# Kernel optimization log

Hardware: AMD Instinct MI355X
Metric: run time of the kernel (lower is better)

Reference implementation:

```python
import jax, jax.numpy as jnp
import numpy as np

N = 50000      # nodes
E = 400000     # edges per hop
IN = 256       # in_channels
H = 4          # heads
C = 64         # out_channels per head
NEG = 0.2      # leaky relu negative slope


def setup_inputs() -> dict:
    key = jax.random.key(0)
    ks = jax.random.split(key, 10)
    x = jax.random.normal(ks[0], (N, IN), dtype=jnp.float32)
    edge_index1 = jax.random.randint(ks[1], (2, E), 0, N, dtype=jnp.int32)
    edge_index2 = jax.random.randint(ks[2], (2, E), 0, N, dtype=jnp.int32)
    s = 0.05
    Wl0 = jax.random.normal(ks[3], (IN, H * C), dtype=jnp.float32) * s
    Wr0 = jax.random.normal(ks[4], (IN, H * C), dtype=jnp.float32) * s
    att0 = jax.random.normal(ks[5], (H, C), dtype=jnp.float32) * s
    Wl1 = jax.random.normal(ks[6], (IN, H * C), dtype=jnp.float32) * s
    Wr1 = jax.random.normal(ks[7], (IN, H * C), dtype=jnp.float32) * s
    att1 = jax.random.normal(ks[8], (H, C), dtype=jnp.float32) * s
    return {"x": x, "Wl0": Wl0, "Wr0": Wr0, "att0": att0,
            "Wl1": Wl1, "Wr1": Wr1, "att1": att1,
            "edge_index1": edge_index1, "edge_index2": edge_index2}


def _gatv2_hop(x, Wl, Wr, att, src, dst):
    """One GATv2Conv hop (bias=False, residual=False, eval-mode dropout, concat=False)."""
    n = x.shape[0]
    xl = (x @ Wl).reshape(n, H, C)   # source-side projection
    xr = (x @ Wr).reshape(n, H, C)   # target-side projection
    # edge-wise GATv2 score: a^T leaky_relu(x_l[j] + x_r[i])
    m = jax.nn.leaky_relu(xl[src] + xr[dst], NEG)            # [E, H, C]
    e = jnp.einsum('ehc,hc->eh', m, att)                     # [E, H]
    # segment softmax over incoming edges of each destination node
    e_max = jax.lax.stop_gradient(
        jax.ops.segment_max(e, dst, num_segments=n))         # [N, H]
    ex = jnp.exp(e - e_max[dst])
    denom = jax.ops.segment_sum(ex, dst, num_segments=n)     # [N, H]
    alpha = ex / (denom[dst] + 1e-16)                        # [E, H]
    msg = xl[src] * alpha[:, :, None]                        # [E, H, C]
    out = jax.ops.segment_sum(msg, dst, num_segments=n)      # [N, H, C]
    return out.mean(axis=1)                                  # concat=False -> mean heads


def reference(x, Wl0, Wr0, att0, Wl1, Wr1, att1, edge_index1, edge_index2):
    n = x.shape[0]
    # hop 0: add_self_loops=True
    loop = jnp.arange(n, dtype=edge_index1.dtype)
    src0 = jnp.concatenate([edge_index1[0], loop])
    dst0 = jnp.concatenate([edge_index1[1], loop])
    out = _gatv2_hop(x, Wl0, Wr0, att0, src0, dst0)
    # hop 1: no self loops, scaled by 1/(k+1) = 1/2
    out = out + _gatv2_hop(x, Wl1, Wr1, att1, edge_index2[0], edge_index2[1]) / 2.0
    return out
```

## Files before the change

### kernel.cpp

```cpp
#include <hip/hip_runtime.h>

typedef unsigned int uint;
typedef unsigned short ushort;

typedef __bf16 bf16x8 __attribute__((ext_vector_type(8)));
typedef float f32x4 __attribute__((ext_vector_type(4)));

#define CAP 48

__device__ __forceinline__ float bf2f(ushort u) {
    return __uint_as_float(((uint)u) << 16);
}
__device__ __forceinline__ ushort f2bf(float f) {
    uint u = __float_as_uint(f);
    u += 0x7fffu + ((u >> 16) & 1u);
    return (ushort)(u >> 16);
}
__device__ __forceinline__ float4 up4(ushort4 v) {
    return make_float4(bf2f(v.x), bf2f(v.y), bf2f(v.z), bf2f(v.w));
}
__device__ __forceinline__ float lrelu(float v) {
    return v > 0.f ? v : 0.2f * v;
}
__device__ __forceinline__ void load_lds16(const ushort* g, ushort* l) {
    __builtin_amdgcn_global_load_lds(
        (const __attribute__((address_space(1))) void*)g,
        (__attribute__((address_space(3))) void*)l, 16, 0, 0);
}
__device__ __forceinline__ int swz(int row) { return (row + (row >> 2)) & 3; }

__global__ __launch_bounds__(256) void prep(
    const float* __restrict__ X, ushort* __restrict__ Xb, int Nrows, int Mpad,
    const float* __restrict__ Wl0, const float* __restrict__ Wr0,
    const float* __restrict__ Wl1, const float* __restrict__ Wr1,
    ushort* __restrict__ Wt,
    int* __restrict__ cnt0, int* __restrict__ srcs0, int* __restrict__ cnt1)
{
    const int BX = Mpad / 8;
    int blk = blockIdx.x;
    if (blk < BX) {
        int i = blk * 256 + threadIdx.x;
        int base = i * 8;
        int row = base >> 8;
        ushort o[8];
        if (row < Nrows) {
            float4 v0 = *(const float4*)(X + base);
            float4 v1 = *(const float4*)(X + base + 4);
            o[0] = f2bf(v0.x); o[1] = f2bf(v0.y); o[2] = f2bf(v0.z); o[3] = f2bf(v0.w);
            o[4] = f2bf(v1.x); o[5] = f2bf(v1.y); o[6] = f2bf(v1.z); o[7] = f2bf(v1.w);
        } else {
#pragma unroll
            for (int j = 0; j < 8; j++) o[j] = 0;
        }
        *(uint4*)(Xb + base) = *(const uint4*)o;
        return;
    }
    blk -= BX;
    if (blk < 1024) {
        int n = blk;
        int k = threadIdx.x;
        const float* W = (n < 256) ? Wl0 : (n < 512) ? Wr0 : (n < 768) ? Wl1 : Wr1;
        Wt[n * 256 + k] = f2bf(W[k * 256 + (n & 255)]);
        return;
    }
    blk -= 1024;
    int d = blk * 256 + threadIdx.x;
    if (d < Nrows) {
        cnt0[d] = 1;
        srcs0[(size_t)d * CAP] = d;
        cnt1[d] = 0;
    }
}

__global__ __launch_bounds__(256) void csr_scatter2(
    const int* __restrict__ ei1, const int* __restrict__ ei2,
    int* __restrict__ cnt0, int* __restrict__ srcs0,
    int* __restrict__ cnt1, int* __restrict__ srcs1,
    int E1, int E2)
{
    int e = blockIdx.x * 256 + threadIdx.x;
    if (e < E1) {
        int d = ei1[E1 + e];
        int pos = atomicAdd(&cnt0[d], 1);
        if (pos < CAP) srcs0[(size_t)d * CAP + pos] = ei1[e];
    } else if (e < E1 + E2) {
        int e2 = e - E1;
        int d = ei2[E2 + e2];
        int pos = atomicAdd(&cnt1[d], 1);
        if (pos < CAP) srcs1[(size_t)d * CAP + pos] = ei2[e2];
    }
}

__global__ __launch_bounds__(256, 2) void gemm_mfma(
    const ushort* __restrict__ Xb,
    const ushort* __restrict__ Wt,
    ushort* __restrict__ XP,
    int Nrows)
{
    __shared__ ushort As[128 * 32];
    __shared__ ushort Bs[128 * 32];

    const int tid = threadIdx.x;
    const int w = tid >> 6, l = tid & 63;
    const int wm = w & 1, wn = w >> 1;
    const int m0 = blockIdx.y * 128;
    const int n0g = blockIdx.x * 128;

    f32x4 acc[4][4];
#pragma unroll
    for (int i = 0; i < 4; i++)
#pragma unroll
        for (int j = 0; j < 4; j++) acc[i][j] = (f32x4)(0.f);

    const int fr = l & 15, fq = l >> 4;
    int a_off[4], b_off[4];
#pragma unroll
    for (int t = 0; t < 4; t++) {
        int rA = wm * 64 + t * 16 + fr;
        a_off[t] = (rA * 4 + ((fq + swz(rA)) & 3)) * 8;
        int rB = wn * 64 + t * 16 + fr;
        b_off[t] = (rB * 4 + ((fq + swz(rB)) & 3)) * 8;
    }

    for (int k0 = 0; k0 < 256; k0 += 32) {
        __syncthreads();
#pragma unroll
        for (int r = 0; r < 2; r++) {
            int slot = r * 256 + tid;
            int row = slot >> 2;
            int kp = ((slot & 3) - swz(row)) & 3;
            load_lds16(Xb + (size_t)(m0 + row) * 256 + k0 + kp * 8,
                       &As[(r * 256 + w * 64) * 8]);
            load_lds16(Wt + (size_t)(n0g + row) * 256 + k0 + kp * 8,
                       &Bs[(r * 256 + w * 64) * 8]);
        }
        __syncthreads();

        bf16x8 a[4], b[4];
#pragma unroll
        for (int t = 0; t < 4; t++) {
            a[t] = *(const bf16x8*)(As + a_off[t]);
            b[t] = *(const bf16x8*)(Bs + b_off[t]);
        }
#pragma unroll
        for (int mi = 0; mi < 4; mi++)
#pragma unroll
            for (int ni = 0; ni < 4; ni++)
                acc[mi][ni] = __builtin_amdgcn_mfma_f32_16x16x32_bf16(
                    a[mi], b[ni], acc[mi][ni], 0, 0, 0);
    }

    ushort* OUT = XP + (size_t)(n0g >> 8) * ((size_t)Nrows * 256);
    const int cbase = (n0g & 255) + wn * 64 + fr;
#pragma unroll
    for (int mi = 0; mi < 4; mi++) {
#pragma unroll
        for (int reg = 0; reg < 4; reg++) {
            int row = m0 + wm * 64 + mi * 16 + fq * 4 + reg;
            if (row >= Nrows) continue;
#pragma unroll
            for (int ni = 0; ni < 4; ni++) {
                OUT[(size_t)row * 256 + cbase + ni * 16] = f2bf(acc[mi][ni][reg]);
            }
        }
    }
}

__device__ __forceinline__ ushort4 gat_load(const ushort* __restrict__ XLb,
                                            int s, int lane) {
    return *(const ushort4*)(XLb + (size_t)s * 256 + lane * 4);
}
__device__ __forceinline__ void edge_accum(ushort4 raw, float4 xr, float4 av,
        float& a0, float& a1, float& a2, float& a3, float& den) {
    float4 xa = up4(raw);
    float p = av.x * lrelu(xa.x + xr.x) + av.y * lrelu(xa.y + xr.y)
            + av.z * lrelu(xa.z + xr.z) + av.w * lrelu(xa.w + xr.w);
    p += __shfl_xor(p, 1);
    p += __shfl_xor(p, 2);
    p += __shfl_xor(p, 4);
    p += __shfl_xor(p, 8);
    float exv = __expf(p);
    den += exv;
    a0 = fmaf(exv, xa.x, a0);
    a1 = fmaf(exv, xa.y, a1);
    a2 = fmaf(exv, xa.z, a2);
    a3 = fmaf(exv, xa.w, a3);
}

__global__ __launch_bounds__(256) void gat_aggregate(
    const ushort* __restrict__ XLb,
    const ushort* __restrict__ XRb,
    const float* __restrict__ att,
    const int* __restrict__ cnt,
    const int* __restrict__ srcs,
    const float* __restrict__ base,
    float* __restrict__ outp,
    float scale, int N)
{
    int d = blockIdx.x * 4 + (threadIdx.x >> 6);
    if (d >= N) return;
    int lane = threadIdx.x & 63;

    float4 xr = up4(*(const ushort4*)(XRb + (size_t)d * 256 + lane * 4));
    float4 av = *(const float4*)(att + lane * 4);

    int m = cnt[d];
    if (m > CAP) m = CAP;
    int sv = (lane < m) ? srcs[(size_t)d * CAP + lane] : 0;

    float a0 = 0.f, a1 = 0.f, a2 = 0.f, a3 = 0.f, den = 0.f;

    if (m > 0) {
        const int c = m - 1;
        ushort4 p[8];
#pragma unroll
        for (int j = 0; j < 8; j++)
            if (j <= c) p[j] = gat_load(XLb, __shfl(sv, j), lane);
        for (int i = 0; i < m; i += 8) {
            ushort4 cur[8];
#pragma unroll
            for (int j = 0; j < 8; j++) cur[j] = p[j];
            int b = i + 8;
#pragma unroll
            for (int j = 0; j < 8; j++)
                if (b + j <= c) p[j] = gat_load(XLb, __shfl(sv, b + j), lane);
#pragma unroll
            for (int j = 0; j < 8; j++)
                if (i + j < m) edge_accum(cur[j], xr, av, a0, a1, a2, a3, den);
        }
    }

    float inv = scale / (den + 1e-16f);
    float v0 = a0 * inv, v1 = a1 * inv, v2 = a2 * inv, v3 = a3 * inv;
    v0 += __shfl_xor(v0, 16); v0 += __shfl_xor(v0, 32);
    v1 += __shfl_xor(v1, 16); v1 += __shfl_xor(v1, 32);
    v2 += __shfl_xor(v2, 16); v2 += __shfl_xor(v2, 32);
    v3 += __shfl_xor(v3, 16); v3 += __shfl_xor(v3, 32);
    int jsel = lane >> 4;
    float vv = (jsel == 0) ? v0 : (jsel == 1) ? v1 : (jsel == 2) ? v2 : v3;
    int ch = ((lane & 15) << 2) + jsel;
    float prev = base ? base[(size_t)d * 64 + ch] : 0.f;
    outp[(size_t)d * 64 + ch] = prev + vv;
}

extern "C" void kernel_launch(void* const* d_in, const int* in_sizes, int n_in,
                              void* d_out, int out_size, void* d_ws, size_t ws_size,
                              hipStream_t stream)
{
    const float* x    = (const float*)d_in[0];
    const float* Wl0  = (const float*)d_in[1];
    const float* Wr0  = (const float*)d_in[2];
    const float* att0 = (const float*)d_in[3];
    const float* Wl1  = (const float*)d_in[4];
    const float* Wr1  = (const float*)d_in[5];
    const float* att1 = (const float*)d_in[6];
    const int* ei1 = (const int*)d_in[7];
    const int* ei2 = (const int*)d_in[8];

    const int N  = in_sizes[0] / 256;
    const int E1 = in_sizes[7] / 2;
    const int E2 = in_sizes[8] / 2;
    const int Mpad = ((N + 127) / 128) * 128;
    const size_t NB = (size_t)N * 256;

    char* ws = (char*)d_ws;
    size_t off = 0;
    ushort* Xb  = (ushort*)(ws + off); off += (size_t)Mpad * 256 * sizeof(ushort);
    ushort* Wt  = (ushort*)(ws + off); off += (size_t)1024 * 256 * sizeof(ushort);
    int* cnt0   = (int*)(ws + off);    off += (size_t)N * sizeof(int);
    int* cnt1   = (int*)(ws + off);    off += (size_t)N * sizeof(int);
    int* srcs0  = (int*)(ws + off);    off += (size_t)N * CAP * sizeof(int);
    int* srcs1  = (int*)(ws + off);    off += (size_t)N * CAP * sizeof(int);
    ushort* XP  = (ushort*)(ws + off);
    size_t need_mega = off + 4 * NB * sizeof(ushort);
    const bool mega = (ws_size >= need_mega);
    float* outf = (float*)d_out;

    const int BX = Mpad / 8;
    int prep_blocks = BX + 1024 + (N + 255) / 256;
    prep<<<prep_blocks, 256, 0, stream>>>(x, Xb, N, Mpad, Wl0, Wr0, Wl1, Wr1,
                                          Wt, cnt0, srcs0, cnt1);
    csr_scatter2<<<(E1 + E2 + 255) / 256, 256, 0, stream>>>(
        ei1, ei2, cnt0, srcs0, cnt1, srcs1, E1, E2);

    int aggblk = (N + 3) / 4;
    if (mega) {
        gemm_mfma<<<dim3(8, Mpad / 128), 256, 0, stream>>>(Xb, Wt, XP, N);
        gat_aggregate<<<aggblk, 256, 0, stream>>>(XP, XP + NB, att0, cnt0, srcs0,
                                                  nullptr, outf, 0.25f, N);
        gat_aggregate<<<aggblk, 256, 0, stream>>>(XP + 2 * NB, XP + 3 * NB, att1,
                                                  cnt1, srcs1, outf, outf, 0.125f, N);
    } else {
        gemm_mfma<<<dim3(4, Mpad / 128), 256, 0, stream>>>(Xb, Wt, XP, N);
        gat_aggregate<<<aggblk, 256, 0, stream>>>(XP, XP + NB, att0, cnt0, srcs0,
                                                  nullptr, outf, 0.25f, N);
        gemm_mfma<<<dim3(4, Mpad / 128), 256, 0, stream>>>(Xb, Wt + 512 * 256, XP, N);
        gat_aggregate<<<aggblk, 256, 0, stream>>>(XP, XP + NB, att1, cnt1, srcs1,
                                                  outf, outf, 0.125f, N);
    }
}
```

Before: 297.9 us.

## Fuse both GAT hops into one aggregation kernel with implicit self-loops

Merges the two per-hop aggregation kernels into a single kernel that computes hop 0 and hop 1 for each destination node and writes the output once. This removes a launch and the read-modify-write of the intermediate output. The self-loop is now handled as an implicit extra edge instead of being stored in the CSR, so hop 0's bucket cap no longer loses a slot to it. Other changes: the prefetch depth drops from 8 to 4 with masked tail edges instead of branches, the edge count is made wave-uniform via readfirstlane, and leaky-ReLU becomes fmax. In exchange, each wave carries more live registers across both hops.

```diff
diff --git a/kernel.cpp b/kernel.cpp
--- a/kernel.cpp
+++ b/kernel.cpp
@@ -18,9 +18,6 @@
 }
 __device__ __forceinline__ float4 up4(ushort4 v) {
     return make_float4(bf2f(v.x), bf2f(v.y), bf2f(v.z), bf2f(v.w));
-}
-__device__ __forceinline__ float lrelu(float v) {
-    return v > 0.f ? v : 0.2f * v;
 }
 __device__ __forceinline__ void load_lds16(const ushort* g, ushort* l) {
     __builtin_amdgcn_global_load_lds(
@@ -34,7 +31,7 @@
     const float* __restrict__ Wl0, const float* __restrict__ Wr0,
     const float* __restrict__ Wl1, const float* __restrict__ Wr1,
     ushort* __restrict__ Wt,
-    int* __restrict__ cnt0, int* __restrict__ srcs0, int* __restrict__ cnt1)
+    int* __restrict__ cnt0, int* __restrict__ cnt1)
 {
     const int BX = Mpad / 8;
     int blk = blockIdx.x;
@@ -66,8 +63,7 @@
     blk -= 1024;
     int d = blk * 256 + threadIdx.x;
     if (d < Nrows) {
-        cnt0[d] = 1;
-        srcs0[(size_t)d * CAP] = d;
+        cnt0[d] = 0;
         cnt1[d] = 0;
     }
 }
@@ -166,72 +162,106 @@
     }
 }
 
-__device__ __forceinline__ ushort4 gat_load(const ushort* __restrict__ XLb,
-                                            int s, int lane) {
-    return *(const ushort4*)(XLb + (size_t)s * 256 + lane * 4);
-}
-__device__ __forceinline__ void edge_accum(ushort4 raw, float4 xr, float4 av,
-        float& a0, float& a1, float& a2, float& a3, float& den) {
-    float4 xa = up4(raw);
-    float p = av.x * lrelu(xa.x + xr.x) + av.y * lrelu(xa.y + xr.y)
-            + av.z * lrelu(xa.z + xr.z) + av.w * lrelu(xa.w + xr.w);
+__device__ __forceinline__ void eacc(ushort4 raw, bool live,
+    const float4& xr, const float4& av,
+    float& a0, float& a1, float& a2, float& a3, float& den)
+{
+    float x0 = bf2f(raw.x), x1 = bf2f(raw.y), x2 = bf2f(raw.z), x3 = bf2f(raw.w);
+    float t0 = x0 + xr.x, t1 = x1 + xr.y, t2 = x2 + xr.z, t3 = x3 + xr.w;
+    float m0 = fmaxf(t0, 0.2f * t0), m1 = fmaxf(t1, 0.2f * t1);
+    float m2 = fmaxf(t2, 0.2f * t2), m3 = fmaxf(t3, 0.2f * t3);
+    float p = av.x * m0;
+    p = fmaf(av.y, m1, p);
+    p = fmaf(av.z, m2, p);
+    p = fmaf(av.w, m3, p);
     p += __shfl_xor(p, 1);
     p += __shfl_xor(p, 2);
     p += __shfl_xor(p, 4);
     p += __shfl_xor(p, 8);
-    float exv = __expf(p);
-    den += exv;
-    a0 = fmaf(exv, xa.x, a0);
-    a1 = fmaf(exv, xa.y, a1);
-    a2 = fmaf(exv, xa.z, a2);
-    a3 = fmaf(exv, xa.w, a3);
-}
-
-__global__ __launch_bounds__(256) void gat_aggregate(
-    const ushort* __restrict__ XLb,
-    const ushort* __restrict__ XRb,
-    const float* __restrict__ att,
-    const int* __restrict__ cnt,
-    const int* __restrict__ srcs,
-    const float* __restrict__ base,
-    float* __restrict__ outp,
-    float scale, int N)
+    float pe = __expf(p);
+    if (!live) pe = 0.f;
+    den += pe;
+    a0 = fmaf(pe, x0, a0);
+    a1 = fmaf(pe, x1, a1);
+    a2 = fmaf(pe, x2, a2);
+    a3 = fmaf(pe, x3, a3);
+}
+
+__device__ __forceinline__ void gat_hop(
+    const ushort* __restrict__ XL, const ushort* __restrict__ XR,
+    const float* __restrict__ att, const int* __restrict__ cnt,
+    const int* __restrict__ srcs, int self, int d, int lane,
+    float& o0, float& o1, float& o2, float& o3)
+{
+    float4 xr = up4(*(const ushort4*)(XR + (size_t)d * 256 + lane * 4));
+    float4 av = *(const float4*)(att + lane * 4);
+
+    int m = __builtin_amdgcn_readfirstlane(cnt[d]);
+    if (m > CAP) m = CAP;
+    const int c = (m > 0) ? (m - 1) : 0;
+    int slot = (lane < m) ? lane : c;
+    int sv = srcs[(size_t)d * CAP + slot];
+
+    float a0 = 0.f, a1 = 0.f, a2 = 0.f, a3 = 0.f, den = 0.f;
+
+    if (self) {
+        ushort4 sr = *(const ushort4*)(XL + (size_t)d * 256 + lane * 4);
+        eacc(sr, true, xr, av, a0, a1, a2, a3, den);
+    }
+    if (m > 0) {
+        ushort4 pf[4];
+#pragma unroll
+        for (int j = 0; j < 4; j++) {
+            int jj = (j < c) ? j : c;
+            int s = __builtin_amdgcn_readlane(sv, jj);
+            pf[j] = *(const ushort4*)(XL + (size_t)s * 256 + lane * 4);
+        }
+        for (int i = 0; i < m; i += 4) {
+            ushort4 c0 = pf[0], c1 = pf[1], c2 = pf[2], c3 = pf[3];
+            int b = i + 4;
+            if (b <= c) {
+#pragma unroll
+                for (int j = 0; j < 4; j++) {
+                    int t = b + j;
+                    int jj = (t < c) ? t : c;
+                    int s = __builtin_amdgcn_readlane(sv, jj);
+                    pf[j] = *(const ushort4*)(XL + (size_t)s * 256 + lane * 4);
+                }
+            }
+            eacc(c0, true,      xr, av, a0, a1, a2, a3, den);
+            eacc(c1, i + 1 < m, xr, av, a0, a1, a2, a3, den);
+            eacc(c2, i + 2 < m, xr, av, a0, a1, a2, a3, den);
+            eacc(c3, i + 3 < m, xr, av, a0, a1, a2, a3, den);
+        }
+    }
+    float inv = 1.f / (den + 1e-16f);
+    o0 = a0 * inv; o1 = a1 * inv; o2 = a2 * inv; o3 = a3 * inv;
+}
+
+__global__ __launch_bounds__(256) void gat_fused(
+    const ushort* __restrict__ XL0, const ushort* __restrict__ XR0,
+    const float* __restrict__ att0,
+    const int* __restrict__ cnt0, const int* __restrict__ srcs0,
+    int self0, float scale0,
+    const ushort* __restrict__ XL1, const ushort* __restrict__ XR1,
+    const float* __restrict__ att1,
+    const int* __restrict__ cnt1, const int* __restrict__ srcs1,
+    float scale1,
+    const float* __restrict__ base, float* __restrict__ outp, int N)
 {
     int d = blockIdx.x * 4 + (threadIdx.x >> 6);
     if (d >= N) return;
     int lane = threadIdx.x & 63;
 
-    float4 xr = up4(*(const ushort4*)(XRb + (size_t)d * 256 + lane * 4));
-    float4 av = *(const float4*)(att + lane * 4);
-
-    int m = cnt[d];
-    if (m > CAP) m = CAP;
-    int sv = (lane < m) ? srcs[(size_t)d * CAP + lane] : 0;
-
-    float a0 = 0.f, a1 = 0.f, a2 = 0.f, a3 = 0.f, den = 0.f;
-
-    if (m > 0) {
-        const int c = m - 1;
-        ushort4 p[8];
-#pragma unroll
-        for (int j = 0; j < 8; j++)
-            if (j <= c) p[j] = gat_load(XLb, __shfl(sv, j), lane);
-        for (int i = 0; i < m; i += 8) {
-            ushort4 cur[8];
-#pragma unroll
-            for (int j = 0; j < 8; j++) cur[j] = p[j];
-            int b = i + 8;
-#pragma unroll
-            for (int j = 0; j < 8; j++)
-                if (b + j <= c) p[j] = gat_load(XLb, __shfl(sv, b + j), lane);
-#pragma unroll
-            for (int j = 0; j < 8; j++)
-                if (i + j < m) edge_accum(cur[j], xr, av, a0, a1, a2, a3, den);
-        }
-    }
-
-    float inv = scale / (den + 1e-16f);
-    float v0 = a0 * inv, v1 = a1 * inv, v2 = a2 * inv, v3 = a3 * inv;
+    float r0, r1, r2, r3;
+    gat_hop(XL0, XR0, att0, cnt0, srcs0, self0, d, lane, r0, r1, r2, r3);
+    float v0 = scale0 * r0, v1 = scale0 * r1, v2 = scale0 * r2, v3 = scale0 * r3;
+    if (cnt1) {
+        float s0, s1, s2, s3;
+        gat_hop(XL1, XR1, att1, cnt1, srcs1, 0, d, lane, s0, s1, s2, s3);
+        v0 = fmaf(scale1, s0, v0); v1 = fmaf(scale1, s1, v1);
+        v2 = fmaf(scale1, s2, v2); v3 = fmaf(scale1, s3, v3);
+    }
     v0 += __shfl_xor(v0, 16); v0 += __shfl_xor(v0, 32);
     v1 += __shfl_xor(v1, 16); v1 += __shfl_xor(v1, 32);
     v2 += __shfl_xor(v2, 16); v2 += __shfl_xor(v2, 32);
@@ -279,23 +309,27 @@
     const int BX = Mpad / 8;
     int prep_blocks = BX + 1024 + (N + 255) / 256;
     prep<<<prep_blocks, 256, 0, stream>>>(x, Xb, N, Mpad, Wl0, Wr0, Wl1, Wr1,
-                                          Wt, cnt0, srcs0, cnt1);
+                                          Wt, cnt0, cnt1);
     csr_scatter2<<<(E1 + E2 + 255) / 256, 256, 0, stream>>>(
         ei1, ei2, cnt0, srcs0, cnt1, srcs1, E1, E2);
 
     int aggblk = (N + 3) / 4;
     if (mega) {
         gemm_mfma<<<dim3(8, Mpad / 128), 256, 0, stream>>>(Xb, Wt, XP, N);
-        gat_aggregate<<<aggblk, 256, 0, stream>>>(XP, XP + NB, att0, cnt0, srcs0,
-                                                  nullptr, outf, 0.25f, N);
-        gat_aggregate<<<aggblk, 256, 0, stream>>>(XP + 2 * NB, XP + 3 * NB, att1,
-                                                  cnt1, srcs1, outf, outf, 0.125f, N);
+        gat_fused<<<aggblk, 256, 0, stream>>>(
+            XP, XP + NB, att0, cnt0, srcs0, 1, 0.25f,
+            XP + 2 * NB, XP + 3 * NB, att1, cnt1, srcs1, 0.125f,
+            nullptr, outf, N);
     } else {
         gemm_mfma<<<dim3(4, Mpad / 128), 256, 0, stream>>>(Xb, Wt, XP, N);
-        gat_aggregate<<<aggblk, 256, 0, stream>>>(XP, XP + NB, att0, cnt0, srcs0,
-                                                  nullptr, outf, 0.25f, N);
+        gat_fused<<<aggblk, 256, 0, stream>>>(
+            XP, XP + NB, att0, cnt0, srcs0, 1, 0.25f,
+            nullptr, nullptr, nullptr, nullptr, nullptr, 0.f,
+            nullptr, outf, N);
         gemm_mfma<<<dim3(4, Mpad / 128), 256, 0, stream>>>(Xb, Wt + 512 * 256, XP, N);
-        gat_aggregate<<<aggblk, 256, 0, stream>>>(XP, XP + NB, att1, cnt1, srcs1,
-                                                  outf, outf, 0.125f, N);
-    }
-}
+        gat_fused<<<aggblk, 256, 0, stream>>>(
+            XP, XP + NB, att1, cnt1, srcs1, 0, 0.125f,
+            nullptr, nullptr, nullptr, nullptr, nullptr, 0.f,
+            outf, outf, N);
+    }
+}
```

Measured after the change: 278.1 us. -6.6%, faster.
